# Optimization experiments

Hardware: AMD Instinct MI355X
Metric: run time of the kernel (lower is better)

## Reference

```python
import jax, jax.numpy as jnp
import numpy as np

# --- DMP / network constants (from init_kwargs) ---
N = 30          # number of RBF basis functions
T = 50          # rollout points returned
L = 10          # integration substeps per rollout point
TAU = 1.0
A_Z = 15.0
A_X = 1.0
DOF = 7         # len(state_index)
SCALE = 1.0     # args.scale
DT = TAU / (T * L)
STEPS = T * L                      # time_steps - 1 = 500
OUT_SIZE = N * DOF + DOF           # 217
B = 4096
D_IN = 64


def setup_inputs() -> dict:
    key = jax.random.key(0)
    ks = jax.random.split(key, 4)
    x = jax.random.normal(ks[0], (B, D_IN), dtype=jnp.float32)
    state = jax.random.normal(ks[1], (B, DOF), dtype=jnp.float32)
    W_pt = jax.random.normal(ks[2], (D_IN, 256), dtype=jnp.float32) * 0.05
    b_pt = jnp.zeros((256,), dtype=jnp.float32)
    W_last = jax.random.normal(ks[3], (256, OUT_SIZE), dtype=jnp.float32) * 0.05
    b_last = jnp.zeros((OUT_SIZE,), dtype=jnp.float32)
    # DMPParameters buffers: c = exp(-a_x * linspace(0,1,N)); sigma2 = N^1.5 / c / a_x
    c_np = np.exp(-A_X * np.linspace(0.0, 1.0, N)).astype(np.float32)
    h_np = (np.ones(N) * N ** 1.5 / c_np / A_X).astype(np.float32)
    return {"x": x, "state": state, "W_pt": W_pt, "b_pt": b_pt,
            "W_last": W_last, "b_last": b_last,
            "c": jnp.asarray(c_np), "h": jnp.asarray(h_np)}


def reference(x, state, W_pt, b_pt, W_last, b_last, c, h):
    # feature net (stand-in for pt.forward_traj), num_layers==1 path
    feat = jnp.tanh(x @ W_pt + b_pt)                      # [B, 256]
    output = (feat @ W_last + b_last) * SCALE             # [B, N*DOF + DOF]

    y0 = state.reshape(-1)                                # [B*DOF]
    dy0 = jnp.ones_like(y0) * 0.05
    goal = output[:, :DOF].reshape(-1)                    # [B*DOF]
    w = output[:, DOF:DOF * (N + 1)].reshape(-1, N)       # [B*DOF, N]

    b_z = A_Z / 4.0
    gy0 = goal - y0                                       # constant forcing scale

    def step(carry, _):
        xp, y, z = carry
        x_new = xp + (-A_X * xp / TAU) * DT               # canonical system
        psi = jnp.exp(-h * (x_new - c) ** 2)              # [N] gaussian RBF
        fx = (w @ psi) * (x_new / jnp.sum(psi)) * gy0     # [B*DOF]
        dz = (A_Z * (b_z * (goal - y) - z) + fx) / TAU
        dy = z / TAU
        y_new = y + dy * DT
        z_new = z + dz * DT
        return (x_new, y_new, z_new), y_new

    init = (jnp.asarray(1.0, dtype=y0.dtype), y0, dy0 * TAU)
    _, Ys = jax.lax.scan(step, init, None, length=STEPS)  # [STEPS, B*DOF]

    Y = jnp.concatenate([y0[None, :], Ys], axis=0).T      # [B*DOF, STEPS+1]
    Y = Y.reshape(state.shape[0], DOF, -1)[:, :, ::L]     # [B, DOF, T+1]
    return jnp.transpose(Y, (0, 2, 1))                    # [B, T+1, DOF]
```

## Files before the change

kernel.cpp:

```cpp
#include <hip/hip_runtime.h>
#include <hip/hip_bf16.h>

#define NB    30
#define TPTS  50
#define DOF   7
#define BATCH 4096
#define DIN   64
#define HID   256
#define OUTC  217
#define STEPS 500
#define DTF   0.002f
#define DTD   0.002
#define AZD   15.0
#define C1D   56.25
#define NELEM (BATCH*DOF)

#define WS_QY     131072
#define WS_QZ     139264
#define WS_CONST  147456
#define WS_WTPT   155648
#define WS_WTLAST 188416

typedef __attribute__((ext_vector_type(8))) short short8;
typedef __attribute__((ext_vector_type(4))) float f32x4;

__device__ __forceinline__ short f2bf(float f) {
  unsigned u = __builtin_bit_cast(unsigned, f);
  unsigned r = (u + 0x7FFFu + ((u >> 16) & 1u)) >> 16;
  return (short)r;
}

__device__ __forceinline__ float tanh_fast(float v) {
  float e = __expf(2.0f * v);
  return 1.0f - __fdividef(2.0f, e + 1.0f);
}

__global__ __launch_bounds__(512) void setup_prep_kernel(
    const float* __restrict__ c, const float* __restrict__ h,
    const float* __restrict__ W_pt, const float* __restrict__ W_last,
    char* __restrict__ ws) {
  const int tid = threadIdx.x;

  if (blockIdx.x == 0) {
    __shared__ float xs[STEPS];
    __shared__ float Pl[STEPS][32];
    float* Qy  = (float*)(ws + WS_QY);
    float* Qz  = (float*)(ws + WS_QZ);
    float* cst = (float*)(ws + WS_CONST);

    if (tid == 0) {
      float x = 1.0f;
      for (int i = 0; i < STEPS; i++) {
        x = x + (-x) * DTF;
        xs[i] = x;
      }
    }
    __syncthreads();

    if (tid < STEPS) {
      const float x = xs[tid];
      float psi[NB];
      float s = 0.0f;
      #pragma unroll
      for (int n = 0; n < NB; n++) {
        float d = x - c[n];
        psi[n] = expf(-h[n] * d * d);
        s += psi[n];
      }
      const float scv = x / s;
      #pragma unroll
      for (int n = 0; n < NB; n++) Pl[tid][n] = psi[n] * scv;
      Pl[tid][30] = 0.0f;
      Pl[tid][31] = 0.0f;
    }
    __syncthreads();

    const double m00 = 1.0, m01 = DTD, m10 = -C1D * DTD, m11 = 1.0 - AZD * DTD;
    double vy[10], vz[10];
    double ay = 0.0, az = 0.0;
    double uy = 0.0, uz = DTD;
    #pragma unroll
    for (int j = 0; j < 10; j++) {
      vy[9 - j] = uy; vz[9 - j] = uz;
      ay += uy; az += uz;
      const double ty = m00 * uy + m01 * uz;
      const double tz = m10 * uy + m11 * uz;
      uy = ty; uz = tz;
    }

    for (int cell = tid; cell < TPTS * 32; cell += 512) {
      const int k = cell >> 5, n = cell & 31;
      double qy = 0.0, qz = 0.0;
      #pragma unroll
      for (int i = 0; i < 10; i++) {
        const double p = (double)Pl[10 * k + i][n];
        qy += p * vy[i];
        qz += p * vz[i];
      }
      Qy[cell] = (float)qy;
      Qz[cell] = (float)qz;
    }

    if (tid == 0) {
      double p00 = 1, p01 = 0, p10 = 0, p11 = 1;
      for (int j = 0; j < 10; j++) {
        const double a2 = m00 * p00 + m01 * p10;
        const double b2 = m00 * p01 + m01 * p11;
        const double c2 = m10 * p00 + m11 * p10;
        const double d2 = m10 * p01 + m11 * p11;
        p00 = a2; p01 = b2; p10 = c2; p11 = d2;
      }
      cst[0] = (float)p00; cst[1] = (float)p01;
      cst[2] = (float)p10; cst[3] = (float)p11;
      cst[4] = (float)(ay * C1D);
      cst[5] = (float)(az * C1D);
      cst[6] = 0.0f; cst[7] = 0.0f;
    }
  } else {
    short* Wt_pt   = (short*)(ws + WS_WTPT);
    short* Wt_last = (short*)(ws + WS_WTLAST);
    const int idx = (blockIdx.x - 1) * 512 + tid;
    if (idx < 256 * 64) {
      const int j = idx >> 6, k = idx & 63;
      Wt_pt[idx] = f2bf(W_pt[k * 256 + j]);
    }
    const int idx2 = idx - 256 * 64;
    if (idx2 >= 0 && idx2 < 224 * 256) {
      const int col = idx2 >> 8, k = idx2 & 255;
      Wt_last[idx2] = (col < OUTC) ? f2bf(W_last[k * OUTC + col]) : (short)0;
    }
  }
}

__global__ __launch_bounds__(256) void mlp_rollout_kernel(
    const float* __restrict__ x,
    const float* __restrict__ state,
    const float* __restrict__ b_pt, const float* __restrict__ b_last,
    const char* __restrict__ ws,
    float* __restrict__ out) {
  const short* Wt_pt   = (const short*)(ws + WS_WTPT);
  const short* Wt_last = (const short*)(ws + WS_WTLAST);
  const float* Qyg     = (const float*)(ws + WS_QY);
  const float* Qzg     = (const float*)(ws + WS_QZ);
  const float* cstg    = (const float*)(ws + WS_CONST);

  __shared__ __align__(16) short feat[16 * 264];
  __shared__ __align__(16) float orow[16][224];
  __shared__ __align__(16) float sQy[TPTS * 32];
  __shared__ __align__(16) float sQz[TPTS * 32];
  __shared__ float sc[8];

  const int tid = threadIdx.x;
  const int w   = tid >> 6;
  const int l   = tid & 63;
  const int lr  = l & 15;
  const int lg  = l >> 4;
  const int row_blk = blockIdx.x * 16;

  {
    const float4* gy = (const float4*)Qyg;
    const float4* gz = (const float4*)Qzg;
    float4* dy = (float4*)sQy;
    float4* dz = (float4*)sQz;
    for (int i = tid; i < 400; i += 256) { dy[i] = gy[i]; dz[i] = gz[i]; }
    if (tid < 8) sc[tid] = cstg[tid];
  }

  short8 a0, a1;
  {
    const float* xr = x + (size_t)(row_blk + lr) * DIN + lg * 8;
    float4 f0 = ((const float4*)xr)[0];
    float4 f1 = ((const float4*)xr)[1];
    float4 g0 = ((const float4*)(xr + 32))[0];
    float4 g1 = ((const float4*)(xr + 32))[1];
    a0[0]=f2bf(f0.x); a0[1]=f2bf(f0.y); a0[2]=f2bf(f0.z); a0[3]=f2bf(f0.w);
    a0[4]=f2bf(f1.x); a0[5]=f2bf(f1.y); a0[6]=f2bf(f1.z); a0[7]=f2bf(f1.w);
    a1[0]=f2bf(g0.x); a1[1]=f2bf(g0.y); a1[2]=f2bf(g0.z); a1[3]=f2bf(g0.w);
    a1[4]=f2bf(g1.x); a1[5]=f2bf(g1.y); a1[6]=f2bf(g1.z); a1[7]=f2bf(g1.w);
  }
  {
    f32x4 accA[4];
    #pragma unroll
    for (int t = 0; t < 4; t++) accA[t] = (f32x4){0.f, 0.f, 0.f, 0.f};
    #pragma unroll
    for (int t = 0; t < 4; t++) {
      const int ct = 4 * w + t;
      short8 b0 = *(const short8*)(Wt_pt + (16 * ct + lr) * 64 + 0  + lg * 8);
      short8 b1 = *(const short8*)(Wt_pt + (16 * ct + lr) * 64 + 32 + lg * 8);
      accA[t] = __builtin_amdgcn_mfma_f32_16x16x32_bf16(a0, b0, accA[t], 0, 0, 0);
      accA[t] = __builtin_amdgcn_mfma_f32_16x16x32_bf16(a1, b1, accA[t], 0, 0, 0);
    }
    #pragma unroll
    for (int t = 0; t < 4; t++) {
      const int col = 16 * (4 * w + t) + lr;
      const float bias = b_pt[col];
      #pragma unroll
      for (int i = 0; i < 4; i++) {
        const int r_loc = lg * 4 + i;
        feat[r_loc * 264 + col] = f2bf(tanh_fast(accA[t][i] + bias));
      }
    }
  }
  __syncthreads();

  {
    f32x4 accB[4];
    #pragma unroll
    for (int t = 0; t < 4; t++) accB[t] = (f32x4){0.f, 0.f, 0.f, 0.f};
    const int nct = (w < 3) ? 4 : 2;
    #pragma unroll
    for (int k0 = 0; k0 < 256; k0 += 32) {
      short8 af = *(const short8*)(feat + lr * 264 + k0 + lg * 8);
      for (int t = 0; t < 4; t++) {
        if (t < nct) {
          const int ct = 4 * w + t;
          short8 bf = *(const short8*)(Wt_last + (16 * ct + lr) * 256 + k0 + lg * 8);
          accB[t] = __builtin_amdgcn_mfma_f32_16x16x32_bf16(af, bf, accB[t], 0, 0, 0);
        }
      }
    }
    for (int t = 0; t < 4; t++) {
      if (t < nct) {
        const int col = 16 * (4 * w + t) + lr;
        const float bias = (col < OUTC) ? b_last[col] : 0.0f;
        #pragma unroll
        for (int i = 0; i < 4; i++) {
          orow[lg * 4 + i][col] = accB[t][i] + bias;
        }
      }
    }
  }
  __syncthreads();

  const int q  = tid & 1;
  const int el = tid >> 1;
  if (el < 112) {
    const int bl = el / DOF;
    const int d  = el - bl * DOF;

    float wq[16];
    #pragma unroll
    for (int j = 0; j < 16; j++) {
      const int n = 16 * q + j;
      wq[j] = (n < NB) ? orow[bl][DOF + d * NB + n] : 0.0f;
    }
    const float goal = orow[bl][d];
    const int eg = (row_blk + bl) * DOF + d;
    float y = state[eg];
    float z = 0.05f;
    const float gy0 = goal - y;

    const float m00 = sc[0], m01 = sc[1], m10 = sc[2], m11 = sc[3];
    const float uy = sc[4] * goal;
    const float uz = sc[5] * goal;

    const int outoff = (row_blk + bl) * ((TPTS + 1) * DOF) + d;
    if (q == 0) out[outoff] = y;

    for (int k = 0; k < TPTS; k++) {
      const float4* qy4 = (const float4*)(sQy + k * 32 + 16 * q);
      const float4* qz4 = (const float4*)(sQz + k * 32 + 16 * q);
      float fy = 0.0f, fz = 0.0f;
      #pragma unroll
      for (int v = 0; v < 4; v++) {
        const float4 ya = qy4[v];
        const float4 za = qz4[v];
        fy = fmaf(wq[4 * v + 0], ya.x, fy);
        fy = fmaf(wq[4 * v + 1], ya.y, fy);
        fy = fmaf(wq[4 * v + 2], ya.z, fy);
        fy = fmaf(wq[4 * v + 3], ya.w, fy);
        fz = fmaf(wq[4 * v + 0], za.x, fz);
        fz = fmaf(wq[4 * v + 1], za.y, fz);
        fz = fmaf(wq[4 * v + 2], za.z, fz);
        fz = fmaf(wq[4 * v + 3], za.w, fz);
      }
      fy += __shfl_xor(fy, 1);
      fz += __shfl_xor(fz, 1);
      const float ny = fmaf(m00, y, fmaf(m01, z, fmaf(gy0, fy, uy)));
      const float nz = fmaf(m10, y, fmaf(m11, z, fmaf(gy0, fz, uz)));
      y = ny; z = nz;
      if (q == 0) out[outoff + (k + 1) * DOF] = y;
    }
  }
}

extern "C" void kernel_launch(void* const* d_in, const int* in_sizes, int n_in,
                              void* d_out, int out_size, void* d_ws, size_t ws_size,
                              hipStream_t stream) {
  const float* x      = (const float*)d_in[0];
  const float* state  = (const float*)d_in[1];
  const float* W_pt   = (const float*)d_in[2];
  const float* b_pt   = (const float*)d_in[3];
  const float* W_last = (const float*)d_in[4];
  const float* b_last = (const float*)d_in[5];
  const float* c      = (const float*)d_in[6];
  const float* h      = (const float*)d_in[7];
  float* out = (float*)d_out;

  char* ws = (char*)d_ws;

  setup_prep_kernel<<<145, 512, 0, stream>>>(c, h, W_pt, W_last, ws);
  mlp_rollout_kernel<<<BATCH / 16, 256, 0, stream>>>(x, state, b_pt, b_last, ws, out);
}
```

Baseline: 99.88 us.

## Fold RBF/propagator table build into main kernel and widen blocks to 512 threads

Moves the per-step basis and propagator table computation out of the serial single-block setup kernel into each block of the main kernel, computed in parallel with powf for the canonical state. This removes the long serial chain in block 0 of the prep kernel, which the main kernel had to wait for. It also doubles the block size to 512 and splits each rollout element's weights across 4 lanes instead of 2. The cost is that every block recomputes the tables redundantly (many expf and double ops). There is also slight numerical drift from powf versus iterated multiplication.

Measured after the change: 92.07 us. 1.08x faster.

```diff
diff --git a/kernel.cpp b/kernel.cpp
--- a/kernel.cpp
+++ b/kernel.cpp
@@ -13,11 +13,7 @@
 #define DTD   0.002
 #define AZD   15.0
 #define C1D   56.25
-#define NELEM (BATCH*DOF)
-
-#define WS_QY     131072
-#define WS_QZ     139264
-#define WS_CONST  147456
+
 #define WS_WTPT   155648
 #define WS_WTLAST 188416
 
@@ -35,119 +31,38 @@
   return 1.0f - __fdividef(2.0f, e + 1.0f);
 }
 
-__global__ __launch_bounds__(512) void setup_prep_kernel(
-    const float* __restrict__ c, const float* __restrict__ h,
+__global__ __launch_bounds__(512) void prep_kernel(
     const float* __restrict__ W_pt, const float* __restrict__ W_last,
     char* __restrict__ ws) {
-  const int tid = threadIdx.x;
-
-  if (blockIdx.x == 0) {
-    __shared__ float xs[STEPS];
-    __shared__ float Pl[STEPS][32];
-    float* Qy  = (float*)(ws + WS_QY);
-    float* Qz  = (float*)(ws + WS_QZ);
-    float* cst = (float*)(ws + WS_CONST);
-
-    if (tid == 0) {
-      float x = 1.0f;
-      for (int i = 0; i < STEPS; i++) {
-        x = x + (-x) * DTF;
-        xs[i] = x;
-      }
-    }
-    __syncthreads();
-
-    if (tid < STEPS) {
-      const float x = xs[tid];
-      float psi[NB];
-      float s = 0.0f;
-      #pragma unroll
-      for (int n = 0; n < NB; n++) {
-        float d = x - c[n];
-        psi[n] = expf(-h[n] * d * d);
-        s += psi[n];
-      }
-      const float scv = x / s;
-      #pragma unroll
-      for (int n = 0; n < NB; n++) Pl[tid][n] = psi[n] * scv;
-      Pl[tid][30] = 0.0f;
-      Pl[tid][31] = 0.0f;
-    }
-    __syncthreads();
-
-    const double m00 = 1.0, m01 = DTD, m10 = -C1D * DTD, m11 = 1.0 - AZD * DTD;
-    double vy[10], vz[10];
-    double ay = 0.0, az = 0.0;
-    double uy = 0.0, uz = DTD;
-    #pragma unroll
-    for (int j = 0; j < 10; j++) {
-      vy[9 - j] = uy; vz[9 - j] = uz;
-      ay += uy; az += uz;
-      const double ty = m00 * uy + m01 * uz;
-      const double tz = m10 * uy + m11 * uz;
-      uy = ty; uz = tz;
-    }
-
-    for (int cell = tid; cell < TPTS * 32; cell += 512) {
-      const int k = cell >> 5, n = cell & 31;
-      double qy = 0.0, qz = 0.0;
-      #pragma unroll
-      for (int i = 0; i < 10; i++) {
-        const double p = (double)Pl[10 * k + i][n];
-        qy += p * vy[i];
-        qz += p * vz[i];
-      }
-      Qy[cell] = (float)qy;
-      Qz[cell] = (float)qz;
-    }
-
-    if (tid == 0) {
-      double p00 = 1, p01 = 0, p10 = 0, p11 = 1;
-      for (int j = 0; j < 10; j++) {
-        const double a2 = m00 * p00 + m01 * p10;
-        const double b2 = m00 * p01 + m01 * p11;
-        const double c2 = m10 * p00 + m11 * p10;
-        const double d2 = m10 * p01 + m11 * p11;
-        p00 = a2; p01 = b2; p10 = c2; p11 = d2;
-      }
-      cst[0] = (float)p00; cst[1] = (float)p01;
-      cst[2] = (float)p10; cst[3] = (float)p11;
-      cst[4] = (float)(ay * C1D);
-      cst[5] = (float)(az * C1D);
-      cst[6] = 0.0f; cst[7] = 0.0f;
-    }
+  short* Wt_pt   = (short*)(ws + WS_WTPT);
+  short* Wt_last = (short*)(ws + WS_WTLAST);
+  const int idx = blockIdx.x * 512 + threadIdx.x;
+  if (idx < 256 * 64) {
+    const int j = idx >> 6, k = idx & 63;
+    Wt_pt[idx] = f2bf(W_pt[k * 256 + j]);
   } else {
-    short* Wt_pt   = (short*)(ws + WS_WTPT);
-    short* Wt_last = (short*)(ws + WS_WTLAST);
-    const int idx = (blockIdx.x - 1) * 512 + tid;
-    if (idx < 256 * 64) {
-      const int j = idx >> 6, k = idx & 63;
-      Wt_pt[idx] = f2bf(W_pt[k * 256 + j]);
-    }
     const int idx2 = idx - 256 * 64;
-    if (idx2 >= 0 && idx2 < 224 * 256) {
-      const int col = idx2 >> 8, k = idx2 & 255;
-      Wt_last[idx2] = (col < OUTC) ? f2bf(W_last[k * OUTC + col]) : (short)0;
-    }
-  }
-}
-
-__global__ __launch_bounds__(256) void mlp_rollout_kernel(
+    const int col = idx2 >> 8, k = idx2 & 255;
+    Wt_last[idx2] = (col < OUTC) ? f2bf(W_last[k * OUTC + col]) : (short)0;
+  }
+}
+
+__global__ __launch_bounds__(512) void fused_kernel(
     const float* __restrict__ x,
     const float* __restrict__ state,
     const float* __restrict__ b_pt, const float* __restrict__ b_last,
+    const float* __restrict__ cbuf, const float* __restrict__ hbuf,
     const char* __restrict__ ws,
     float* __restrict__ out) {
   const short* Wt_pt   = (const short*)(ws + WS_WTPT);
   const short* Wt_last = (const short*)(ws + WS_WTLAST);
-  const float* Qyg     = (const float*)(ws + WS_QY);
-  const float* Qzg     = (const float*)(ws + WS_QZ);
-  const float* cstg    = (const float*)(ws + WS_CONST);
 
   __shared__ __align__(16) short feat[16 * 264];
   __shared__ __align__(16) float orow[16][224];
   __shared__ __align__(16) float sQy[TPTS * 32];
   __shared__ __align__(16) float sQz[TPTS * 32];
+  __shared__ float xs[STEPS];
+  __shared__ float inv[STEPS];
   __shared__ float sc[8];
 
   const int tid = threadIdx.x;
@@ -157,13 +72,72 @@
   const int lg  = l >> 4;
   const int row_blk = blockIdx.x * 16;
 
+  if (tid < STEPS) {
+    const float xv = powf(1.0f - DTF, (float)(tid + 1));
+    float s = 0.0f;
+    #pragma unroll
+    for (int n = 0; n < NB; n++) {
+      const float d = xv - cbuf[n];
+      s += expf(-hbuf[n] * d * d);
+    }
+    xs[tid] = xv;
+    inv[tid] = xv / s;
+  }
+  if (tid == 0) {
+    const double m00 = 1.0, m01 = DTD, m10 = -C1D * DTD, m11 = 1.0 - AZD * DTD;
+    double ay = 0.0, az = 0.0;
+    double uy = 0.0, uz = DTD;
+    double p00 = 1, p01 = 0, p10 = 0, p11 = 1;
+    for (int j = 0; j < 10; j++) {
+      ay += uy; az += uz;
+      const double ty = m00 * uy + m01 * uz;
+      const double tz = m10 * uy + m11 * uz;
+      uy = ty; uz = tz;
+      const double a2 = m00 * p00 + m01 * p10;
+      const double b2 = m00 * p01 + m01 * p11;
+      const double c2 = m10 * p00 + m11 * p10;
+      const double d2 = m10 * p01 + m11 * p11;
+      p00 = a2; p01 = b2; p10 = c2; p11 = d2;
+    }
+    sc[0] = (float)p00; sc[1] = (float)p01;
+    sc[2] = (float)p10; sc[3] = (float)p11;
+    sc[4] = (float)(ay * C1D);
+    sc[5] = (float)(az * C1D);
+    sc[6] = 0.0f; sc[7] = 0.0f;
+  }
+  __syncthreads();
+
   {
-    const float4* gy = (const float4*)Qyg;
-    const float4* gz = (const float4*)Qzg;
-    float4* dy = (float4*)sQy;
-    float4* dz = (float4*)sQz;
-    for (int i = tid; i < 400; i += 256) { dy[i] = gy[i]; dz[i] = gz[i]; }
-    if (tid < 8) sc[tid] = cstg[tid];
+    const double m00 = 1.0, m01 = DTD, m10 = -C1D * DTD, m11 = 1.0 - AZD * DTD;
+    double vy[10], vz[10];
+    double uy = 0.0, uz = DTD;
+    #pragma unroll
+    for (int j = 0; j < 10; j++) {
+      vy[9 - j] = uy; vz[9 - j] = uz;
+      const double ty = m00 * uy + m01 * uz;
+      const double tz = m10 * uy + m11 * uz;
+      uy = ty; uz = tz;
+    }
+    for (int cell = tid; cell < TPTS * 32; cell += 512) {
+      const int k = cell >> 5, n = cell & 31;
+      float qyf = 0.0f, qzf = 0.0f;
+      if (n < NB) {
+        const float cn = cbuf[n], hn = hbuf[n];
+        double qy = 0.0, qz = 0.0;
+        #pragma unroll
+        for (int i = 0; i < 10; i++) {
+          const int t = 10 * k + i;
+          const float xv = xs[t];
+          const float d = xv - cn;
+          const float p = expf(-hn * d * d) * inv[t];
+          qy += (double)p * vy[i];
+          qz += (double)p * vz[i];
+        }
+        qyf = (float)qy; qzf = (float)qz;
+      }
+      sQy[cell] = qyf;
+      sQz[cell] = qzf;
+    }
   }
 
   short8 a0, a1;
@@ -179,69 +153,65 @@
     a1[4]=f2bf(g1.x); a1[5]=f2bf(g1.y); a1[6]=f2bf(g1.z); a1[7]=f2bf(g1.w);
   }
   {
-    f32x4 accA[4];
-    #pragma unroll
-    for (int t = 0; t < 4; t++) accA[t] = (f32x4){0.f, 0.f, 0.f, 0.f};
-    #pragma unroll
-    for (int t = 0; t < 4; t++) {
-      const int ct = 4 * w + t;
+    f32x4 accA[2];
+    #pragma unroll
+    for (int t = 0; t < 2; t++) accA[t] = (f32x4){0.f, 0.f, 0.f, 0.f};
+    #pragma unroll
+    for (int t = 0; t < 2; t++) {
+      const int ct = 2 * w + t;
       short8 b0 = *(const short8*)(Wt_pt + (16 * ct + lr) * 64 + 0  + lg * 8);
       short8 b1 = *(const short8*)(Wt_pt + (16 * ct + lr) * 64 + 32 + lg * 8);
       accA[t] = __builtin_amdgcn_mfma_f32_16x16x32_bf16(a0, b0, accA[t], 0, 0, 0);
       accA[t] = __builtin_amdgcn_mfma_f32_16x16x32_bf16(a1, b1, accA[t], 0, 0, 0);
     }
     #pragma unroll
-    for (int t = 0; t < 4; t++) {
-      const int col = 16 * (4 * w + t) + lr;
+    for (int t = 0; t < 2; t++) {
+      const int col = 16 * (2 * w + t) + lr;
       const float bias = b_pt[col];
       #pragma unroll
       for (int i = 0; i < 4; i++) {
-        const int r_loc = lg * 4 + i;
-        feat[r_loc * 264 + col] = f2bf(tanh_fast(accA[t][i] + bias));
+        feat[(lg * 4 + i) * 264 + col] = f2bf(tanh_fast(accA[t][i] + bias));
       }
     }
   }
   __syncthreads();
 
-  {
-    f32x4 accB[4];
-    #pragma unroll
-    for (int t = 0; t < 4; t++) accB[t] = (f32x4){0.f, 0.f, 0.f, 0.f};
-    const int nct = (w < 3) ? 4 : 2;
+  if (w < 7) {
+    f32x4 accB[2];
+    #pragma unroll
+    for (int t = 0; t < 2; t++) accB[t] = (f32x4){0.f, 0.f, 0.f, 0.f};
     #pragma unroll
     for (int k0 = 0; k0 < 256; k0 += 32) {
       short8 af = *(const short8*)(feat + lr * 264 + k0 + lg * 8);
-      for (int t = 0; t < 4; t++) {
-        if (t < nct) {
-          const int ct = 4 * w + t;
-          short8 bf = *(const short8*)(Wt_last + (16 * ct + lr) * 256 + k0 + lg * 8);
-          accB[t] = __builtin_amdgcn_mfma_f32_16x16x32_bf16(af, bf, accB[t], 0, 0, 0);
-        }
-      }
-    }
-    for (int t = 0; t < 4; t++) {
-      if (t < nct) {
-        const int col = 16 * (4 * w + t) + lr;
-        const float bias = (col < OUTC) ? b_last[col] : 0.0f;
-        #pragma unroll
-        for (int i = 0; i < 4; i++) {
-          orow[lg * 4 + i][col] = accB[t][i] + bias;
-        }
+      #pragma unroll
+      for (int t = 0; t < 2; t++) {
+        const int ct = 2 * w + t;
+        short8 bf = *(const short8*)(Wt_last + (16 * ct + lr) * 256 + k0 + lg * 8);
+        accB[t] = __builtin_amdgcn_mfma_f32_16x16x32_bf16(af, bf, accB[t], 0, 0, 0);
+      }
+    }
+    #pragma unroll
+    for (int t = 0; t < 2; t++) {
+      const int col = 16 * (2 * w + t) + lr;
+      const float bias = (col < OUTC) ? b_last[col] : 0.0f;
+      #pragma unroll
+      for (int i = 0; i < 4; i++) {
+        orow[lg * 4 + i][col] = accB[t][i] + bias;
       }
     }
   }
   __syncthreads();
 
-  const int q  = tid & 1;
-  const int el = tid >> 1;
+  const int q  = tid & 3;
+  const int el = tid >> 2;
   if (el < 112) {
     const int bl = el / DOF;
     const int d  = el - bl * DOF;
 
-    float wq[16];
-    #pragma unroll
-    for (int j = 0; j < 16; j++) {
-      const int n = 16 * q + j;
+    float wq[8];
+    #pragma unroll
+    for (int j = 0; j < 8; j++) {
+      const int n = 8 * q + j;
       wq[j] = (n < NB) ? orow[bl][DOF + d * NB + n] : 0.0f;
     }
     const float goal = orow[bl][d];
@@ -254,32 +224,31 @@
     const float uy = sc[4] * goal;
     const float uz = sc[5] * goal;
 
-    const int outoff = (row_blk + bl) * ((TPTS + 1) * DOF) + d;
-    if (q == 0) out[outoff] = y;
+    const int outoff = eg * (TPTS + 1) - eg + eg;
+    const int outbase = (row_blk + bl) * ((TPTS + 1) * DOF) + d;
+    (void)outoff;
+    if (q == 0) out[outbase] = y;
 
     for (int k = 0; k < TPTS; k++) {
-      const float4* qy4 = (const float4*)(sQy + k * 32 + 16 * q);
-      const float4* qz4 = (const float4*)(sQz + k * 32 + 16 * q);
+      const float4* qy4 = (const float4*)(sQy + k * 32 + 8 * q);
+      const float4* qz4 = (const float4*)(sQz + k * 32 + 8 * q);
+      const float4 ya = qy4[0], yb = qy4[1];
+      const float4 za = qz4[0], zb = qz4[1];
       float fy = 0.0f, fz = 0.0f;
-      #pragma unroll
-      for (int v = 0; v < 4; v++) {
-        const float4 ya = qy4[v];
-        const float4 za = qz4[v];
-        fy = fmaf(wq[4 * v + 0], ya.x, fy);
-        fy = fmaf(wq[4 * v + 1], ya.y, fy);
-        fy = fmaf(wq[4 * v + 2], ya.z, fy);
-        fy = fmaf(wq[4 * v + 3], ya.w, fy);
-        fz = fmaf(wq[4 * v + 0], za.x, fz);
-        fz = fmaf(wq[4 * v + 1], za.y, fz);
-        fz = fmaf(wq[4 * v + 2], za.z, fz);
-        fz = fmaf(wq[4 * v + 3], za.w, fz);
-      }
-      fy += __shfl_xor(fy, 1);
-      fz += __shfl_xor(fz, 1);
+      fy = fmaf(wq[0], ya.x, fy); fy = fmaf(wq[1], ya.y, fy);
+      fy = fmaf(wq[2], ya.z, fy); fy = fmaf(wq[3], ya.w, fy);
+      fy = fmaf(wq[4], yb.x, fy); fy = fmaf(wq[5], yb.y, fy);
+      fy = fmaf(wq[6], yb.z, fy); fy = fmaf(wq[7], yb.w, fy);
+      fz = fmaf(wq[0], za.x, fz); fz = fmaf(wq[1], za.y, fz);
+      fz = fmaf(wq[2], za.z, fz); fz = fmaf(wq[3], za.w, fz);
+      fz = fmaf(wq[4], zb.x, fz); fz = fmaf(wq[5], zb.y, fz);
+      fz = fmaf(wq[6], zb.z, fz); fz = fmaf(wq[7], zb.w, fz);
+      fy += __shfl_xor(fy, 1); fy += __shfl_xor(fy, 2);
+      fz += __shfl_xor(fz, 1); fz += __shfl_xor(fz, 2);
       const float ny = fmaf(m00, y, fmaf(m01, z, fmaf(gy0, fy, uy)));
       const float nz = fmaf(m10, y, fmaf(m11, z, fmaf(gy0, fz, uz)));
       y = ny; z = nz;
-      if (q == 0) out[outoff + (k + 1) * DOF] = y;
+      if (q == 0) out[outbase + (k + 1) * DOF] = y;
     }
   }
 }
@@ -299,6 +268,6 @@
 
   char* ws = (char*)d_ws;
 
-  setup_prep_kernel<<<145, 512, 0, stream>>>(c, h, W_pt, W_last, ws);
-  mlp_rollout_kernel<<<BATCH / 16, 256, 0, stream>>>(x, state, b_pt, b_last, ws, out);
-}
+  prep_kernel<<<144, 512, 0, stream>>>(W_pt, W_last, ws);
+  fused_kernel<<<BATCH / 16, 512, 0, stream>>>(x, state, b_pt, b_last, c, h, ws, out);
+}
```
